# Optimization experiments

Hardware: AMD Instinct MI355X
Metric: run time of the kernel (lower is better)

## Reference

```python
import jax, jax.numpy as jnp
import numpy as np

SIZE = (160, 192, 224)  # (D, H, W)


def setup_inputs() -> dict:
    key = jax.random.key(0)
    k1, k2 = jax.random.split(key)
    src = jax.random.normal(k1, (2, 1) + SIZE, dtype=jnp.float32)
    flow = jax.random.normal(k2, (2, 3) + SIZE, dtype=jnp.float32)
    return {"src": src, "flow": flow}


def _warp3d(src, flow):
    # src: [B, C, D, H, W]; flow: [B, 3, D, H, W] (voxel displacements, (d,h,w) order)
    # Equivalent to: normalize (grid+flow) to [-1,1], permute/flip, then
    # F.grid_sample(align_corners=True, mode='bilinear', padding_mode='zeros').
    # The normalization and grid_sample's un-normalization cancel exactly, so we
    # sample src at voxel coords grid+flow with trilinear interp, zeros padding.
    B, C, D, H, W = src.shape
    dt = src.dtype
    gd, gh, gw = jnp.meshgrid(
        jnp.arange(D, dtype=dt), jnp.arange(H, dtype=dt), jnp.arange(W, dtype=dt),
        indexing="ij")
    cd = gd[None] + flow[:, 0]  # [B, D, H, W]
    ch = gh[None] + flow[:, 1]
    cw = gw[None] + flow[:, 2]

    d0f = jnp.floor(cd); h0f = jnp.floor(ch); w0f = jnp.floor(cw)
    fd = cd - d0f; fh = ch - h0f; fw = cw - w0f  # fractional weights
    d0 = d0f.astype(jnp.int32); h0 = h0f.astype(jnp.int32); w0 = w0f.astype(jnp.int32)

    src_flat = src.reshape(B, C, D * H * W)
    out = jnp.zeros((B, C, D, H, W), dt)
    for dd in (0, 1):
        wd = fd if dd else (1.0 - fd)
        idd = d0 + dd
        for hh in (0, 1):
            wh = fh if hh else (1.0 - fh)
            ihh = h0 + hh
            for ww in (0, 1):
                wwt = fw if ww else (1.0 - fw)
                iww = w0 + ww
                valid = ((idd >= 0) & (idd < D) & (ihh >= 0) & (ihh < H)
                         & (iww >= 0) & (iww < W)).astype(dt)
                lin = ((jnp.clip(idd, 0, D - 1) * H + jnp.clip(ihh, 0, H - 1)) * W
                       + jnp.clip(iww, 0, W - 1))  # [B, D, H, W]
                vals = jnp.take_along_axis(
                    src_flat, lin.reshape(B, 1, -1), axis=2).reshape(B, C, D, H, W)
                out = out + vals * (wd * wh * wwt * valid)[:, None]
    return out


def reference(src, flow):
    return _warp3d(src, flow)
```

## Files before the change

kernel.cpp:

```cpp
#include <hip/hip_runtime.h>


#define DD 160
#define HH 192
#define WW 224
constexpr int DHW = DD * HH * WW;
constexpr int BLOCK = 512;
constexpr int DT = DD / 16;
constexpr int HT = HH / 8;
constexpr int WT = WW / 16;
constexpr int BRICKS_PER_B = DT * HT * WT;
constexpr int NWG = 2 * BRICKS_PER_B;
constexpr int NXCD = 8;
constexpr int CHUNK = NWG / NXCD;

constexpr int RD = 24, RH = 16, RWE = 24, RWS = 24;
constexpr int TILE_N = RD * RH * RWS;
constexpr int SROWS = RD * RH;
constexpr int SCHUNKS = SROWS * 6;
constexpr int WCHUNKS = SCHUNKS / 8;
constexpr int DROW = RH * RWS;

typedef float vfloat4 __attribute__((ext_vector_type(4)));

__device__ __forceinline__ float trilerp_global(const float* __restrict__ sbase,
                                                float cd, float ch, float cw) {
    float d0f = floorf(cd), h0f = floorf(ch), w0f = floorf(cw);
    float fd = cd - d0f, fh = ch - h0f, fw = cw - w0f;
    int d0 = (int)d0f, h0 = (int)h0f, w0 = (int)w0f;
    int d1 = d0 + 1, h1 = h0 + 1, w1 = w0 + 1;

    float wd0 = (1.0f - fd) * ((unsigned)d0 < (unsigned)DD ? 1.0f : 0.0f);
    float wd1 = fd          * ((unsigned)d1 < (unsigned)DD ? 1.0f : 0.0f);
    float wh0 = (1.0f - fh) * ((unsigned)h0 < (unsigned)HH ? 1.0f : 0.0f);
    float wh1 = fh          * ((unsigned)h1 < (unsigned)HH ? 1.0f : 0.0f);
    float ww0 = (1.0f - fw) * ((unsigned)w0 < (unsigned)WW ? 1.0f : 0.0f);
    float ww1 = fw          * ((unsigned)w1 < (unsigned)WW ? 1.0f : 0.0f);

    int d0c = min(max(d0, 0), DD - 1), d1c = min(max(d1, 0), DD - 1);
    int h0c = min(max(h0, 0), HH - 1), h1c = min(max(h1, 0), HH - 1);
    int w0c = min(max(w0, 0), WW - 1), w1c = min(max(w1, 0), WW - 1);

    const float* p00 = sbase + (d0c * HH + h0c) * WW;
    const float* p01 = sbase + (d0c * HH + h1c) * WW;
    const float* p10 = sbase + (d1c * HH + h0c) * WW;
    const float* p11 = sbase + (d1c * HH + h1c) * WW;

    return wd0 * (wh0 * (ww0 * p00[w0c] + ww1 * p00[w1c]) +
                  wh1 * (ww0 * p01[w0c] + ww1 * p01[w1c])) +
           wd1 * (wh0 * (ww0 * p10[w0c] + ww1 * p10[w1c]) +
                  wh1 * (ww0 * p11[w0c] + ww1 * p11[w1c]));
}

__global__ __launch_bounds__(512, 8) void warp3d_kernel(
    const float* __restrict__ src, const float* __restrict__ flow,
    float* __restrict__ out) {
    __shared__ __align__(16) float tile[TILE_N];

    int bid = blockIdx.x;
    int wg  = (bid & 7) * CHUNK + (bid >> 3);

    int b  = wg / BRICKS_PER_B;
    int r  = wg - b * BRICKS_PER_B;
    int dt = r / (HT * WT);
    int r2 = r - dt * (HT * WT);
    int ht = r2 / WT;
    int wtile = r2 - ht * WT;

    int dB = dt * 16, hB = ht * 8, wB = wtile * 16;
    int dB4 = dB - 4, hB4 = hB - 4, wB4 = wB - 4;

    bool interior = (dt >= 1) & (dt <= DT - 2) & (ht >= 1) & (ht <= HT - 2)
                  & (wtile >= 1) & (wtile <= WT - 2);

    const float* sbase = src + (size_t)b * DHW;

    int tid  = threadIdx.x;
    int wave = tid >> 6;
    int lane = tid & 63;
    int d = dB + (wave >> 1) * 4 + (lane >> 4);
    int h = hB + (wave & 1) * 4 + ((lane >> 2) & 3);
    int w = wB + (lane & 3) * 4;

    size_t sOff = (size_t)(d * HH + h) * WW + w;
    const float* fb = flow + (size_t)b * 3 * DHW + sOff;
    vfloat4 fld = *reinterpret_cast<const vfloat4*>(fb);
    vfloat4 flh = *reinterpret_cast<const vfloat4*>(fb + DHW);
    vfloat4 flw = *reinterpret_cast<const vfloat4*>(fb + 2 * DHW);

    bool wedge = (wtile == 0) | (wtile == WT - 1);
    if (!wedge) {
        int wbase = wave * WCHUNKS;
        #pragma unroll
        for (int it = 0; it < 5; ++it) {
            int u = wbase + it * 64 + lane;
            if (u < SCHUNKS) {
                int row = u / 6;
                int c   = u - row * 6;
                int ld = row >> 4, lh = row & 15;
                int dg = min(max(dB4 + ld, 0), DD - 1);
                int hg = min(max(hB4 + lh, 0), HH - 1);
                const float* gsrc = sbase + (size_t)(dg * HH + hg) * WW
                                  + (wB4 + 4 * c);
                __builtin_amdgcn_global_load_lds(
                    (const __attribute__((address_space(1))) unsigned int*)gsrc,
                    (__attribute__((address_space(3))) unsigned int*)
                        &tile[(size_t)(wbase + it * 64) * 4],
                    16, 0, 0);
            }
        }
    } else {
        for (int u = tid; u < SCHUNKS; u += BLOCK) {
            int row = u / 6;
            int c   = u - row * 6;
            int ld = row >> 4, lh = row & 15;
            int dg = min(max(dB4 + ld, 0), DD - 1);
            int hg = min(max(hB4 + lh, 0), HH - 1);
            const float* grow = sbase + (size_t)(dg * HH + hg) * WW;
            int wg0 = wB4 + 4 * c;
            vfloat4 v;
            v.x = grow[min(max(wg0 + 0, 0), WW - 1)];
            v.y = grow[min(max(wg0 + 1, 0), WW - 1)];
            v.z = grow[min(max(wg0 + 2, 0), WW - 1)];
            v.w = grow[min(max(wg0 + 3, 0), WW - 1)];
            *reinterpret_cast<vfloat4*>(&tile[u * 4]) = v;
        }
    }

    float df = (float)d, hf = (float)h, wf = (float)w;
    float fdv[4] = {fld.x, fld.y, fld.z, fld.w};
    float fhv[4] = {flh.x, flh.y, flh.z, flh.w};
    float fwv[4] = {flw.x, flw.y, flw.z, flw.w};

    float fdq[4], fhq[4], fwq[4];
    int   base[4];
    bool  okv[4];
    #pragma unroll
    for (int k = 0; k < 4; ++k) {
        float cd = df + fdv[k], ch = hf + fhv[k], cw = wf + (float)k + fwv[k];
        float d0f = floorf(cd), h0f = floorf(ch), w0f = floorf(cw);
        fdq[k] = cd - d0f; fhq[k] = ch - h0f; fwq[k] = cw - w0f;
        int rd = (int)d0f - dB4, rh = (int)h0f - hB4, rw = (int)w0f - wB4;
        okv[k] = ((unsigned)rd < (unsigned)(RD - 1)) &
                 ((unsigned)rh < (unsigned)(RH - 1)) &
                 ((unsigned)rw < (unsigned)(RWE - 1));
        base[k] = (rd * RH + rh) * RWS + rw;
    }
    bool allin = okv[0] & okv[1] & okv[2] & okv[3];

    __syncthreads();

    float res[4];
    if (allin) {
        if (interior) {
            #pragma unroll
            for (int k = 0; k < 4; ++k) {
                int b0 = base[k];
                float fw = fwq[k], fh = fhq[k], fd = fdq[k];
                float v0 = tile[b0],                 v1 = tile[b0 + 1];
                float v2 = tile[b0 + RWS],           v3 = tile[b0 + RWS + 1];
                float v4 = tile[b0 + DROW],          v5 = tile[b0 + DROW + 1];
                float v6 = tile[b0 + DROW + RWS];
                float v7 = tile[b0 + DROW + RWS + 1];
                float x0 = fmaf(fw, v1 - v0, v0);
                float x1 = fmaf(fw, v3 - v2, v2);
                float x2 = fmaf(fw, v5 - v4, v4);
                float x3 = fmaf(fw, v7 - v6, v6);
                float y0 = fmaf(fh, x1 - x0, x0);
                float y1 = fmaf(fh, x3 - x2, x2);
                res[k] = fmaf(fd, y1 - y0, y0);
            }
        } else {
            #pragma unroll
            for (int k = 0; k < 4; ++k) {
                float cd = df + fdv[k], ch = hf + fhv[k],
                      cw = wf + (float)k + fwv[k];
                int d0 = (int)floorf(cd), h0 = (int)floorf(ch),
                    w0 = (int)floorf(cw);
                float fd = fdq[k], fh = fhq[k], fw = fwq[k];
                float wd0 = (1.0f - fd) * ((unsigned)d0 < (unsigned)DD ? 1.0f : 0.0f);
                float wd1 = fd    * ((unsigned)(d0 + 1) < (unsigned)DD ? 1.0f : 0.0f);
                float wh0 = (1.0f - fh) * ((unsigned)h0 < (unsigned)HH ? 1.0f : 0.0f);
                float wh1 = fh    * ((unsigned)(h0 + 1) < (unsigned)HH ? 1.0f : 0.0f);
                float ww0 = (1.0f - fw) * ((unsigned)w0 < (unsigned)WW ? 1.0f : 0.0f);
                float ww1 = fw    * ((unsigned)(w0 + 1) < (unsigned)WW ? 1.0f : 0.0f);
                int b0 = base[k];
                float v0 = tile[b0],                 v1 = tile[b0 + 1];
                float v2 = tile[b0 + RWS],           v3 = tile[b0 + RWS + 1];
                float v4 = tile[b0 + DROW],          v5 = tile[b0 + DROW + 1];
                float v6 = tile[b0 + DROW + RWS];
                float v7 = tile[b0 + DROW + RWS + 1];
                float a = wd0 * wh0, bq = wd0 * wh1, cq = wd1 * wh0, dq = wd1 * wh1;
                res[k] = a  * (ww0 * v0 + ww1 * v1) + bq * (ww0 * v2 + ww1 * v3) +
                         cq * (ww0 * v4 + ww1 * v5) + dq * (ww0 * v6 + ww1 * v7);
            }
        }
    } else {
        #pragma unroll
        for (int k = 0; k < 4; ++k)
            res[k] = trilerp_global(sbase, df + fdv[k], hf + fhv[k],
                                    wf + (float)k + fwv[k]);
    }

    vfloat4 o4 = {res[0], res[1], res[2], res[3]};
    *reinterpret_cast<vfloat4*>(out + (size_t)b * DHW + sOff) = o4;
}

extern "C" void kernel_launch(void* const* d_in, const int* in_sizes, int n_in,
                              void* d_out, int out_size, void* d_ws, size_t ws_size,
                              hipStream_t stream) {
    const float* src  = (const float*)d_in[0];
    const float* flow = (const float*)d_in[1];
    float* out = (float*)d_out;

    warp3d_kernel<<<NWG, BLOCK, 0, stream>>>(src, flow, out);
}
```

Measured before the change: 75.46 us.

## Process two depth bricks per workgroup with double-buffered LDS and partial waitcnt

Each workgroup now handles two 16-deep bricks stacked along depth. Both bricks' halo tiles are issued as async global-to-LDS loads up front. A partial vmcnt wait lets the first brick be computed while the second tile is still in flight. This halves the grid and amortizes launch and address setup. It doubles LDS per block and lowers the occupancy hint from 8 to 4. The hand-counted vmcnt values depend on the compiler's instruction ordering, which could race if that ordering changes.

```diff
diff --git a/kernel.cpp b/kernel.cpp
--- a/kernel.cpp
+++ b/kernel.cpp
@@ -6,11 +6,11 @@
 #define WW 224
 constexpr int DHW = DD * HH * WW;
 constexpr int BLOCK = 512;
-constexpr int DT = DD / 16;
+constexpr int QT = DD / 32;
 constexpr int HT = HH / 8;
 constexpr int WT = WW / 16;
-constexpr int BRICKS_PER_B = DT * HT * WT;
-constexpr int NWG = 2 * BRICKS_PER_B;
+constexpr int PAIRS_PER_B = QT * HT * WT;
+constexpr int NWG = 2 * PAIRS_PER_B;
 constexpr int NXCD = 8;
 constexpr int CHUNK = NWG / NXCD;
 
@@ -52,116 +52,36 @@
                   wh1 * (ww0 * p11[w0c] + ww1 * p11[w1c]));
 }
 
-__global__ __launch_bounds__(512, 8) void warp3d_kernel(
-    const float* __restrict__ src, const float* __restrict__ flow,
-    float* __restrict__ out) {
-    __shared__ __align__(16) float tile[TILE_N];
-
-    int bid = blockIdx.x;
-    int wg  = (bid & 7) * CHUNK + (bid >> 3);
-
-    int b  = wg / BRICKS_PER_B;
-    int r  = wg - b * BRICKS_PER_B;
-    int dt = r / (HT * WT);
-    int r2 = r - dt * (HT * WT);
-    int ht = r2 / WT;
-    int wtile = r2 - ht * WT;
-
-    int dB = dt * 16, hB = ht * 8, wB = wtile * 16;
-    int dB4 = dB - 4, hB4 = hB - 4, wB4 = wB - 4;
-
-    bool interior = (dt >= 1) & (dt <= DT - 2) & (ht >= 1) & (ht <= HT - 2)
-                  & (wtile >= 1) & (wtile <= WT - 2);
-
-    const float* sbase = src + (size_t)b * DHW;
-
-    int tid  = threadIdx.x;
-    int wave = tid >> 6;
-    int lane = tid & 63;
-    int d = dB + (wave >> 1) * 4 + (lane >> 4);
-    int h = hB + (wave & 1) * 4 + ((lane >> 2) & 3);
-    int w = wB + (lane & 3) * 4;
-
-    size_t sOff = (size_t)(d * HH + h) * WW + w;
-    const float* fb = flow + (size_t)b * 3 * DHW + sOff;
-    vfloat4 fld = *reinterpret_cast<const vfloat4*>(fb);
-    vfloat4 flh = *reinterpret_cast<const vfloat4*>(fb + DHW);
-    vfloat4 flw = *reinterpret_cast<const vfloat4*>(fb + 2 * DHW);
-
-    bool wedge = (wtile == 0) | (wtile == WT - 1);
-    if (!wedge) {
-        int wbase = wave * WCHUNKS;
-        #pragma unroll
-        for (int it = 0; it < 5; ++it) {
-            int u = wbase + it * 64 + lane;
-            if (u < SCHUNKS) {
-                int row = u / 6;
-                int c   = u - row * 6;
-                int ld = row >> 4, lh = row & 15;
-                int dg = min(max(dB4 + ld, 0), DD - 1);
-                int hg = min(max(hB4 + lh, 0), HH - 1);
-                const float* gsrc = sbase + (size_t)(dg * HH + hg) * WW
-                                  + (wB4 + 4 * c);
-                __builtin_amdgcn_global_load_lds(
-                    (const __attribute__((address_space(1))) unsigned int*)gsrc,
-                    (__attribute__((address_space(3))) unsigned int*)
-                        &tile[(size_t)(wbase + it * 64) * 4],
-                    16, 0, 0);
-            }
-        }
-    } else {
-        for (int u = tid; u < SCHUNKS; u += BLOCK) {
-            int row = u / 6;
-            int c   = u - row * 6;
-            int ld = row >> 4, lh = row & 15;
-            int dg = min(max(dB4 + ld, 0), DD - 1);
-            int hg = min(max(hB4 + lh, 0), HH - 1);
-            const float* grow = sbase + (size_t)(dg * HH + hg) * WW;
-            int wg0 = wB4 + 4 * c;
-            vfloat4 v;
-            v.x = grow[min(max(wg0 + 0, 0), WW - 1)];
-            v.y = grow[min(max(wg0 + 1, 0), WW - 1)];
-            v.z = grow[min(max(wg0 + 2, 0), WW - 1)];
-            v.w = grow[min(max(wg0 + 3, 0), WW - 1)];
-            *reinterpret_cast<vfloat4*>(&tile[u * 4]) = v;
-        }
-    }
-
-    float df = (float)d, hf = (float)h, wf = (float)w;
-    float fdv[4] = {fld.x, fld.y, fld.z, fld.w};
-    float fhv[4] = {flh.x, flh.y, flh.z, flh.w};
-    float fwv[4] = {flw.x, flw.y, flw.z, flw.w};
-
+__device__ __forceinline__ void compute_brick(
+    const float* __restrict__ tb, const float* __restrict__ sbase,
+    int dB4, int hB4, int wB4,
+    const float* cdv, const float* chv, const float* cwv,
+    bool interior, float* res) {
     float fdq[4], fhq[4], fwq[4];
-    int   base[4];
-    bool  okv[4];
+    int base[4];
+    bool allin = true;
     #pragma unroll
     for (int k = 0; k < 4; ++k) {
-        float cd = df + fdv[k], ch = hf + fhv[k], cw = wf + (float)k + fwv[k];
+        float cd = cdv[k], ch = chv[k], cw = cwv[k];
         float d0f = floorf(cd), h0f = floorf(ch), w0f = floorf(cw);
         fdq[k] = cd - d0f; fhq[k] = ch - h0f; fwq[k] = cw - w0f;
         int rd = (int)d0f - dB4, rh = (int)h0f - hB4, rw = (int)w0f - wB4;
-        okv[k] = ((unsigned)rd < (unsigned)(RD - 1)) &
-                 ((unsigned)rh < (unsigned)(RH - 1)) &
-                 ((unsigned)rw < (unsigned)(RWE - 1));
+        allin = allin & ((unsigned)rd < (unsigned)(RD - 1)) &
+                        ((unsigned)rh < (unsigned)(RH - 1)) &
+                        ((unsigned)rw < (unsigned)(RWE - 1));
         base[k] = (rd * RH + rh) * RWS + rw;
     }
-    bool allin = okv[0] & okv[1] & okv[2] & okv[3];
-
-    __syncthreads();
-
-    float res[4];
     if (allin) {
         if (interior) {
             #pragma unroll
             for (int k = 0; k < 4; ++k) {
                 int b0 = base[k];
                 float fw = fwq[k], fh = fhq[k], fd = fdq[k];
-                float v0 = tile[b0],                 v1 = tile[b0 + 1];
-                float v2 = tile[b0 + RWS],           v3 = tile[b0 + RWS + 1];
-                float v4 = tile[b0 + DROW],          v5 = tile[b0 + DROW + 1];
-                float v6 = tile[b0 + DROW + RWS];
-                float v7 = tile[b0 + DROW + RWS + 1];
+                float v0 = tb[b0],               v1 = tb[b0 + 1];
+                float v2 = tb[b0 + RWS],         v3 = tb[b0 + RWS + 1];
+                float v4 = tb[b0 + DROW],        v5 = tb[b0 + DROW + 1];
+                float v6 = tb[b0 + DROW + RWS];
+                float v7 = tb[b0 + DROW + RWS + 1];
                 float x0 = fmaf(fw, v1 - v0, v0);
                 float x1 = fmaf(fw, v3 - v2, v2);
                 float x2 = fmaf(fw, v5 - v4, v4);
@@ -173,10 +93,8 @@
         } else {
             #pragma unroll
             for (int k = 0; k < 4; ++k) {
-                float cd = df + fdv[k], ch = hf + fhv[k],
-                      cw = wf + (float)k + fwv[k];
-                int d0 = (int)floorf(cd), h0 = (int)floorf(ch),
-                    w0 = (int)floorf(cw);
+                int d0 = (int)floorf(cdv[k]), h0 = (int)floorf(chv[k]),
+                    w0 = (int)floorf(cwv[k]);
                 float fd = fdq[k], fh = fhq[k], fw = fwq[k];
                 float wd0 = (1.0f - fd) * ((unsigned)d0 < (unsigned)DD ? 1.0f : 0.0f);
                 float wd1 = fd    * ((unsigned)(d0 + 1) < (unsigned)DD ? 1.0f : 0.0f);
@@ -185,11 +103,11 @@
                 float ww0 = (1.0f - fw) * ((unsigned)w0 < (unsigned)WW ? 1.0f : 0.0f);
                 float ww1 = fw    * ((unsigned)(w0 + 1) < (unsigned)WW ? 1.0f : 0.0f);
                 int b0 = base[k];
-                float v0 = tile[b0],                 v1 = tile[b0 + 1];
-                float v2 = tile[b0 + RWS],           v3 = tile[b0 + RWS + 1];
-                float v4 = tile[b0 + DROW],          v5 = tile[b0 + DROW + 1];
-                float v6 = tile[b0 + DROW + RWS];
-                float v7 = tile[b0 + DROW + RWS + 1];
+                float v0 = tb[b0],               v1 = tb[b0 + 1];
+                float v2 = tb[b0 + RWS],         v3 = tb[b0 + RWS + 1];
+                float v4 = tb[b0 + DROW],        v5 = tb[b0 + DROW + 1];
+                float v6 = tb[b0 + DROW + RWS];
+                float v7 = tb[b0 + DROW + RWS + 1];
                 float a = wd0 * wh0, bq = wd0 * wh1, cq = wd1 * wh0, dq = wd1 * wh1;
                 res[k] = a  * (ww0 * v0 + ww1 * v1) + bq * (ww0 * v2 + ww1 * v3) +
                          cq * (ww0 * v4 + ww1 * v5) + dq * (ww0 * v6 + ww1 * v7);
@@ -198,12 +116,158 @@
     } else {
         #pragma unroll
         for (int k = 0; k < 4; ++k)
-            res[k] = trilerp_global(sbase, df + fdv[k], hf + fhv[k],
-                                    wf + (float)k + fwv[k]);
+            res[k] = trilerp_global(sbase, cdv[k], chv[k], cwv[k]);
     }
-
-    vfloat4 o4 = {res[0], res[1], res[2], res[3]};
-    *reinterpret_cast<vfloat4*>(out + (size_t)b * DHW + sOff) = o4;
+}
+
+__global__ __launch_bounds__(512, 4) void warp3d_kernel(
+    const float* __restrict__ src, const float* __restrict__ flow,
+    float* __restrict__ out) {
+    __shared__ __align__(16) float tile[2][TILE_N];
+
+    int bid = blockIdx.x;
+    int wg  = (bid & 7) * CHUNK + (bid >> 3);
+
+    int b  = wg / PAIRS_PER_B;
+    int r  = wg - b * PAIRS_PER_B;
+    int q  = r / (HT * WT);
+    int r2 = r - q * (HT * WT);
+    int ht = r2 / WT;
+    int wtile = r2 - ht * WT;
+
+    int dB0 = q * 32, hB = ht * 8, wB = wtile * 16;
+    int dB4_0 = dB0 - 4, dB4_1 = dB0 + 12, hB4 = hB - 4, wB4 = wB - 4;
+
+    bool hwok = (ht >= 1) & (ht <= HT - 2) & (wtile >= 1) & (wtile <= WT - 2);
+    bool interior0 = hwok & (q >= 1);
+    bool interior1 = hwok & (q <= QT - 2);
+    bool wedge = (wtile == 0) | (wtile == WT - 1);
+
+    const float* sbase = src + (size_t)b * DHW;
+
+    int tid  = threadIdx.x;
+    int wave = tid >> 6;
+    int lane = tid & 63;
+    int d = dB0 + (wave >> 1) * 4 + (lane >> 4);
+    int h = hB + (wave & 1) * 4 + ((lane >> 2) & 3);
+    int w = wB + (lane & 3) * 4;
+
+    size_t sOff0 = (size_t)(d * HH + h) * WW + w;
+    size_t sOff1 = sOff0 + (size_t)16 * HH * WW;
+    const float* fb = flow + (size_t)b * 3 * DHW;
+
+    vfloat4 fld0 = *reinterpret_cast<const vfloat4*>(fb + sOff0);
+    vfloat4 flh0 = *reinterpret_cast<const vfloat4*>(fb + DHW + sOff0);
+    vfloat4 flw0 = *reinterpret_cast<const vfloat4*>(fb + 2 * DHW + sOff0);
+    vfloat4 fld1 = *reinterpret_cast<const vfloat4*>(fb + sOff1);
+    vfloat4 flh1 = *reinterpret_cast<const vfloat4*>(fb + DHW + sOff1);
+    vfloat4 flw1 = *reinterpret_cast<const vfloat4*>(fb + 2 * DHW + sOff1);
+
+    float df0 = (float)d, df1 = (float)(d + 16);
+    float hf = (float)h, wf = (float)w;
+
+    float cdv0[4], chv0[4], cwv0[4], cdv1[4], chv1[4], cwv1[4];
+    float res0[4], res1[4];
+
+    if (!wedge) {
+        #pragma unroll
+        for (int bk = 0; bk < 2; ++bk) {
+            int dB4x = bk ? dB4_1 : dB4_0;
+            float* buf = &tile[bk][0];
+            int wbase = wave * WCHUNKS;
+            #pragma unroll
+            for (int it = 0; it < 5; ++it) {
+                int u = wbase + it * 64 + lane;
+                if (u < SCHUNKS) {
+                    int row = u / 6;
+                    int c   = u - row * 6;
+                    int ld = row >> 4, lh = row & 15;
+                    int dg = min(max(dB4x + ld, 0), DD - 1);
+                    int hg = min(max(hB4 + lh, 0), HH - 1);
+                    const float* gsrc = sbase + (size_t)(dg * HH + hg) * WW
+                                      + (wB4 + 4 * c);
+                    __builtin_amdgcn_global_load_lds(
+                        (const __attribute__((address_space(1))) unsigned int*)gsrc,
+                        (__attribute__((address_space(3))) unsigned int*)
+                            &buf[(size_t)(wbase + it * 64) * 4],
+                        16, 0, 0);
+                }
+            }
+        }
+
+        #pragma unroll
+        for (int k = 0; k < 4; ++k) {
+            cdv0[k] = df0 + fld0[k];
+            chv0[k] = hf + flh0[k];
+            cwv0[k] = wf + (float)k + flw0[k];
+        }
+
+        asm volatile("s_waitcnt vmcnt(5)" ::: "memory");
+        __builtin_amdgcn_sched_barrier(0);
+        __builtin_amdgcn_s_barrier();
+
+        compute_brick(&tile[0][0], sbase, dB4_0, hB4, wB4,
+                      cdv0, chv0, cwv0, interior0, res0);
+        vfloat4 o0 = {res0[0], res0[1], res0[2], res0[3]};
+        *reinterpret_cast<vfloat4*>(out + (size_t)b * DHW + sOff0) = o0;
+
+        #pragma unroll
+        for (int k = 0; k < 4; ++k) {
+            cdv1[k] = df1 + fld1[k];
+            chv1[k] = hf + flh1[k];
+            cwv1[k] = wf + (float)k + flw1[k];
+        }
+
+        asm volatile("s_waitcnt vmcnt(1)" ::: "memory");
+        __builtin_amdgcn_sched_barrier(0);
+        __builtin_amdgcn_s_barrier();
+
+        compute_brick(&tile[1][0], sbase, dB4_1, hB4, wB4,
+                      cdv1, chv1, cwv1, interior1, res1);
+        vfloat4 o1 = {res1[0], res1[1], res1[2], res1[3]};
+        *reinterpret_cast<vfloat4*>(out + (size_t)b * DHW + sOff1) = o1;
+    } else {
+        #pragma unroll
+        for (int bk = 0; bk < 2; ++bk) {
+            int dB4x = bk ? dB4_1 : dB4_0;
+            float* buf = &tile[bk][0];
+            for (int u = tid; u < SCHUNKS; u += BLOCK) {
+                int row = u / 6;
+                int c   = u - row * 6;
+                int ld = row >> 4, lh = row & 15;
+                int dg = min(max(dB4x + ld, 0), DD - 1);
+                int hg = min(max(hB4 + lh, 0), HH - 1);
+                const float* grow = sbase + (size_t)(dg * HH + hg) * WW;
+                int wg0 = wB4 + 4 * c;
+                vfloat4 v;
+                v.x = grow[min(max(wg0 + 0, 0), WW - 1)];
+                v.y = grow[min(max(wg0 + 1, 0), WW - 1)];
+                v.z = grow[min(max(wg0 + 2, 0), WW - 1)];
+                v.w = grow[min(max(wg0 + 3, 0), WW - 1)];
+                *reinterpret_cast<vfloat4*>(&buf[u * 4]) = v;
+            }
+        }
+        #pragma unroll
+        for (int k = 0; k < 4; ++k) {
+            cdv0[k] = df0 + fld0[k];
+            chv0[k] = hf + flh0[k];
+            cwv0[k] = wf + (float)k + flw0[k];
+            cdv1[k] = df1 + fld1[k];
+            chv1[k] = hf + flh1[k];
+            cwv1[k] = wf + (float)k + flw1[k];
+        }
+        __syncthreads();
+
+        compute_brick(&tile[0][0], sbase, dB4_0, hB4, wB4,
+                      cdv0, chv0, cwv0, interior0, res0);
+        vfloat4 o0 = {res0[0], res0[1], res0[2], res0[3]};
+        *reinterpret_cast<vfloat4*>(out + (size_t)b * DHW + sOff0) = o0;
+
+        compute_brick(&tile[1][0], sbase, dB4_1, hB4, wB4,
+                      cdv1, chv1, cwv1, interior1, res1);
+        vfloat4 o1 = {res1[0], res1[1], res1[2], res1[3]};
+        *reinterpret_cast<vfloat4*>(out + (size_t)b * DHW + sOff1) = o1;
+    }
 }
 
 extern "C" void kernel_launch(void* const* d_in, const int* in_sizes, int n_in,
```

Measured after the change: 82.33 us. 1.09x slower.
